# Performance work log

Measured on AMD Instinct MI355X. Metric: run time of the kernel, lower is better.

Reference implementation:

```python
import jax, jax.numpy as jnp
import numpy as np
import math

D_MODEL = 1024
NUM_HEADS = 16
D_K = D_MODEL // NUM_HEADS  # 64
THETA = 10000.0
B, S = 2, 2048


def setup_inputs() -> dict:
    key = jax.random.key(0)
    kx, kq, kk, kv, ko = jax.random.split(key, 5)
    sigma = (2.0 / (D_MODEL + D_MODEL)) ** 0.5
    return {
        "x": jax.random.normal(kx, (B, S, D_MODEL), dtype=jnp.float32),
        "Wq": jax.random.normal(kq, (D_MODEL, D_MODEL), dtype=jnp.float32) * sigma,
        "Wk": jax.random.normal(kk, (D_MODEL, D_MODEL), dtype=jnp.float32) * sigma,
        "Wv": jax.random.normal(kv, (D_MODEL, D_MODEL), dtype=jnp.float32) * sigma,
        "Wo": jax.random.normal(ko, (D_MODEL, D_MODEL), dtype=jnp.float32) * sigma,
        "token_positions": jnp.arange(S, dtype=jnp.int32),
    }


def _rope(x, token_positions):
    # x: [..., seq, d_k]; rotate interleaved even/odd pairs.
    half = x.shape[-1] // 2
    freq = jnp.power(THETA, -jnp.arange(0, x.shape[-1], 2, dtype=jnp.float32) / x.shape[-1])  # [half]
    angles = token_positions[:, None].astype(jnp.float32) * freq[None, :]  # [seq, half]
    cos, sin = jnp.cos(angles), jnp.sin(angles)
    x1 = x[..., 0::2]
    x2 = x[..., 1::2]
    out = jnp.stack([x1 * cos - x2 * sin, x1 * sin + x2 * cos], axis=-1)  # [..., seq, half, 2]
    return out.reshape(x.shape)


def reference(x, Wq, Wk, Wv, Wo, token_positions):
    Bb, Ss, Dm = x.shape
    H, Dk = NUM_HEADS, D_K
    # Linear: y = x @ W.T ; split as (n head) -> heads first
    def heads(y):
        return y.reshape(Bb, Ss, H, Dk).transpose(0, 2, 1, 3)  # [B,H,S,Dk]
    Q = heads(x @ Wq.T)
    K = heads(x @ Wk.T)
    V = heads(x @ Wv.T)
    Q = _rope(Q, token_positions)
    K = _rope(K, token_positions)
    scores = jnp.einsum("bhqd,bhkd->bhqk", Q, K) / math.sqrt(Dk)  # [B,H,S,S]
    causal = jnp.tril(jnp.ones((Ss, Ss), dtype=bool))
    scores = jnp.where(causal, scores, -jnp.inf)
    # original casts to fp64 for softmax; numerically-stable fp32 softmax here
    probs = jax.nn.softmax(scores, axis=-1)
    attn = jnp.einsum("bhqk,bhkd->bhqd", probs, V)  # [B,H,S,Dk]
    attn = attn.transpose(0, 2, 1, 3).reshape(Bb, Ss, Dm)
    return attn @ Wo.T
```

## Files before the change

### kernel.cpp

```cpp
#include <hip/hip_runtime.h>
#include <hip/hip_bf16.h>
#include <math.h>

typedef __bf16 bf16_t;
typedef __attribute__((ext_vector_type(8))) __bf16 bf16x8;
typedef __attribute__((ext_vector_type(4))) __bf16 bf16x4;
typedef __attribute__((ext_vector_type(4))) float f32x4;

#define B_DIM 2
#define S_DIM 2048
#define H_DIM 16
#define DK 64
#define DM 1024
#define KDIM 1024

#define MFMA(a, b, c) __builtin_amdgcn_mfma_f32_16x16x32_bf16((a), (b), (c), 0, 0, 0)

__device__ __forceinline__ void gload_lds16(const bf16_t* g, bf16_t* l) {
    __builtin_amdgcn_global_load_lds(
        (const __attribute__((address_space(1))) void*)g,
        (__attribute__((address_space(3))) void*)l, 16, 0, 0);
}

__global__ void cvt_all(const float* __restrict__ x,
                        const float* __restrict__ wq, const float* __restrict__ wk,
                        const float* __restrict__ wv, const float* __restrict__ wo,
                        bf16_t* __restrict__ xb,
                        bf16_t* __restrict__ wqb, bf16_t* __restrict__ wkb,
                        bf16_t* __restrict__ wvb, bf16_t* __restrict__ wob) {
    const long NX = (long)B_DIM * S_DIM * DM;
    const long i = ((long)blockIdx.x * 256 + threadIdx.x) * 4;
    const float* s; bf16_t* d; long off;
    if (i < NX) { s = x; d = xb; off = i; }
    else {
        const long j = i - NX;
        const int wsel = (int)(j >> 20);
        off = j & ((1L << 20) - 1);
        switch (wsel) {
            case 0: s = wq; d = wqb; break;
            case 1: s = wk; d = wkb; break;
            case 2: s = wv; d = wvb; break;
            default: s = wo; d = wob; break;
        }
    }
    float4 v = *reinterpret_cast<const float4*>(s + off);
    bf16x4 o;
    o[0] = (__bf16)v.x; o[1] = (__bf16)v.y; o[2] = (__bf16)v.z; o[3] = (__bf16)v.w;
    *reinterpret_cast<bf16x4*>(d + off) = o;
}

template <int MODE>
__global__ __launch_bounds__(256)
void gemm_bt(const bf16_t* __restrict__ A,
             const bf16_t* __restrict__ B0,
             const bf16_t* __restrict__ B1,
             const bf16_t* __restrict__ B2,
             bf16_t* __restrict__ outQ,
             bf16_t* __restrict__ outK,
             bf16_t* __restrict__ outVt,
             float* __restrict__ outF,
             const int* __restrict__ pos) {
    constexpr int CP = 136;
    constexpr int SELEMS = (MODE == 0) ? (128 * CP) : 16384;
    __shared__ bf16_t smem[SELEMS];
    bf16_t* As = smem;
    bf16_t* Bs = smem + 8192;
    bf16_t* Cs = smem;

    const int t = threadIdx.x;
    const int z = blockIdx.z;
    const bf16_t* Bm = (MODE == 0) ? (z == 0 ? B0 : (z == 1 ? B1 : B2)) : B0;

    const int m0 = blockIdx.x * 128;
    const int n0 = blockIdx.y * 128;
    const int lane = t & 63;
    const int w = t >> 6;
    const int wr = w >> 1;
    const int wc = w & 1;

    f32x4 acc[4][4] = {};

    const bf16_t* Ag = A + (size_t)m0 * KDIM;
    const bf16_t* Bg = Bm + (size_t)n0 * KDIM;

    const int rr = lane & 15;
    const int ko = (lane >> 4) * 8;

    int rI[4], cI[4];
#pragma unroll
    for (int c = 0; c < 4; ++c) {
        const int i = t + c * 256;
        rI[c] = i >> 3;
        cI[c] = ((i & 7) ^ (rI[c] & 7)) * 8;
    }

    for (int k0 = 0; k0 < KDIM; k0 += 64) {
#pragma unroll
        for (int c = 0; c < 4; ++c) {
            const int i = t + c * 256;
            gload_lds16(Ag + (size_t)rI[c] * KDIM + k0 + cI[c], &As[i * 8]);
        }
#pragma unroll
        for (int c = 0; c < 4; ++c) {
            const int i = t + c * 256;
            gload_lds16(Bg + (size_t)rI[c] * KDIM + k0 + cI[c], &Bs[i * 8]);
        }
        __syncthreads();

        bf16x8 af[2][4], bfr[2][4];
#pragma unroll
        for (int kk = 0; kk < 2; ++kk) {
#pragma unroll
            for (int m = 0; m < 4; ++m) {
                const int r = wr * 64 + m * 16 + rr;
                af[kk][m] = *reinterpret_cast<const bf16x8*>(
                    &As[r * 64 + ((kk * 32 + ko) ^ ((r & 7) * 8))]);
            }
#pragma unroll
            for (int n = 0; n < 4; ++n) {
                const int r = wc * 64 + n * 16 + rr;
                bfr[kk][n] = *reinterpret_cast<const bf16x8*>(
                    &Bs[r * 64 + ((kk * 32 + ko) ^ ((r & 7) * 8))]);
            }
        }
        __builtin_amdgcn_s_setprio(1);
#pragma unroll
        for (int kk = 0; kk < 2; ++kk)
#pragma unroll
            for (int m = 0; m < 4; ++m)
#pragma unroll
                for (int n = 0; n < 4; ++n)
                    acc[m][n] = MFMA(af[kk][m], bfr[kk][n], acc[m][n]);
        __builtin_amdgcn_s_setprio(0);
        __syncthreads();
    }

    const int rlb = wr * 64 + (lane >> 4) * 4;
    const int clb = wc * 64 + (lane & 15);

    if (MODE == 0) {
        if (z < 2) {
#pragma unroll
            for (int m = 0; m < 4; ++m)
#pragma unroll
                for (int n = 0; n < 4; ++n)
#pragma unroll
                    for (int j = 0; j < 4; ++j)
                        Cs[(rlb + m * 16 + j) * CP + clb + n * 16] = (__bf16)acc[m][n][j];
            __syncthreads();

            bf16_t* dst = (z == 0) ? outQ : outK;
            const int dch = t & 7;
            const int srow = t >> 3;
            float fr[4];
#pragma unroll
            for (int i = 0; i < 4; ++i)
                fr[i] = exp2f((float)(dch * 4 + i) * -0.4152410118609203f);
#pragma unroll
            for (int p = 0; p < 4; ++p) {
                const int s_loc = p * 32 + srow;
                const int gm = m0 + s_loc;
                const int bb = gm >> 11, sg = gm & (S_DIM - 1);
                const float pv = (float)pos[sg];
                float csv[4], snv[4];
#pragma unroll
                for (int i = 0; i < 4; ++i) {
                    const float a = pv * fr[i];
                    csv[i] = cosf(a); snv[i] = sinf(a);
                }
#pragma unroll
                for (int hc = 0; hc < 2; ++hc) {
                    const bf16x8 vv = *reinterpret_cast<const bf16x8*>(
                        &Cs[s_loc * CP + hc * 64 + dch * 8]);
                    bf16x8 ov;
#pragma unroll
                    for (int i = 0; i < 4; ++i) {
                        const float v0 = (float)vv[2 * i], v1 = (float)vv[2 * i + 1];
                        ov[2 * i]     = (__bf16)(v0 * csv[i] - v1 * snv[i]);
                        ov[2 * i + 1] = (__bf16)(v0 * snv[i] + v1 * csv[i]);
                    }
                    const int h = (n0 >> 6) + hc;
                    *reinterpret_cast<bf16x8*>(
                        &dst[((size_t)(bb * H_DIM + h) * S_DIM + sg) * 64 + dch * 8]) = ov;
                }
            }
        } else {
#pragma unroll
            for (int m = 0; m < 4; ++m)
#pragma unroll
                for (int n = 0; n < 4; ++n) {
                    const int cl = clb + n * 16;
                    bf16x4 v4;
#pragma unroll
                    for (int j = 0; j < 4; ++j) v4[j] = (__bf16)acc[m][n][j];
                    *reinterpret_cast<bf16x4*>(&Cs[cl * CP + rlb + m * 16]) = v4;
                }
            __syncthreads();

            const int cl = t >> 1, sh = t & 1;
            const int cg = n0 + cl, h = cg >> 6, d = cg & 63;
            const int bb = m0 >> 11, s0g = m0 & (S_DIM - 1);
            bf16_t* vdst = &outVt[((size_t)(bb * H_DIM + h) * DK + d) * S_DIM + s0g + sh * 64];
#pragma unroll
            for (int i = 0; i < 8; ++i)
                *reinterpret_cast<bf16x8*>(&vdst[i * 8]) =
                    *reinterpret_cast<const bf16x8*>(&Cs[cl * CP + sh * 64 + i * 8]);
        }
    } else {
        const int rbase = m0 + rlb;
        const int cbase = n0 + clb;
#pragma unroll
        for (int m = 0; m < 4; ++m)
#pragma unroll
            for (int n = 0; n < 4; ++n)
#pragma unroll
                for (int j = 0; j < 4; ++j)
                    outF[(size_t)(rbase + m * 16 + j) * DM + cbase + n * 16] = acc[m][n][j];
    }
}

__global__ __launch_bounds__(256, 4)
void attn_kernel(const bf16_t* __restrict__ Q, const bf16_t* __restrict__ Kg,
                 const bf16_t* __restrict__ Vt, bf16_t* __restrict__ O) {
    __shared__ bf16_t Ks[2][64 * 64];
    __shared__ bf16_t Vs[2][64 * 64];
    __shared__ bf16_t P_lds[4][16 * 64];

    const int t = threadIdx.x;
    const int lane = t & 63;
    const int w = t >> 6;
    const int qbo = blockIdx.x >> 5;
    const int qb = 31 - qbo;
    const int bh = blockIdx.x & 31;
    const int q0 = qb * 64 + w * 16;
    const int b = bh >> 4, h = bh & 15;
    const int rr = lane & 15;
    const int hi = lane >> 4;
    const int psw = (rr & 7) * 8;

    const bf16_t* Kbh = Kg + (size_t)bh * S_DIM * DK;
    const bf16_t* Vbh = Vt + (size_t)bh * DK * S_DIM;
    bf16_t* Pw = P_lds[w];

    const int i0 = t, i1 = t + 256;
    const int r0 = i0 >> 3, c0 = ((i0 & 7) ^ (r0 & 7)) * 8;
    const int r1 = i1 >> 3, c1 = ((i1 & 7) ^ (r1 & 7)) * 8;

    const float QSCALE = 0.18033688011112042f;
    const bf16_t* Qp = Q + ((size_t)bh * S_DIM + q0) * DK;
    bf16x8 qf[2];
    qf[0] = *reinterpret_cast<const bf16x8*>(&Qp[rr * DK + hi * 8]);
    qf[1] = *reinterpret_cast<const bf16x8*>(&Qp[rr * DK + 32 + hi * 8]);
#pragma unroll
    for (int i = 0; i < 8; ++i) {
        qf[0][i] = (__bf16)((float)qf[0][i] * QSCALE);
        qf[1][i] = (__bf16)((float)qf[1][i] * QSCALE);
    }

    bf16x8 ones;
#pragma unroll
    for (int i = 0; i < 8; ++i) ones[i] = (__bf16)1.0f;

    f32x4 o[4] = {};
    f32x4 la = {};
    float m = -INFINITY;

    const int nt = qb + 1;

    gload_lds16(Kbh + (size_t)r0 * DK + c0, &Ks[0][i0 * 8]);
    gload_lds16(Kbh + (size_t)r1 * DK + c1, &Ks[0][i1 * 8]);
    gload_lds16(Vbh + (size_t)r0 * S_DIM + c0, &Vs[0][i0 * 8]);
    gload_lds16(Vbh + (size_t)r1 * S_DIM + c1, &Vs[0][i1 * 8]);
    __syncthreads();

    for (int tt = 0; tt < nt; ++tt) {
        const int cur = tt & 1;
        const int kv0 = tt * 64;

        if (tt + 1 < nt) {
            const int kv1 = kv0 + 64;
            bf16_t* Kn = Ks[cur ^ 1];
            bf16_t* Vn = Vs[cur ^ 1];
            gload_lds16(Kbh + (size_t)(kv1 + r0) * DK + c0, &Kn[i0 * 8]);
            gload_lds16(Kbh + (size_t)(kv1 + r1) * DK + c1, &Kn[i1 * 8]);
            gload_lds16(Vbh + (size_t)r0 * S_DIM + kv1 + c0, &Vn[i0 * 8]);
            gload_lds16(Vbh + (size_t)r1 * S_DIM + kv1 + c1, &Vn[i1 * 8]);
        }
        const bf16_t* Kc = Ks[cur];
        const bf16_t* Vc = Vs[cur];

        f32x4 s[4] = {};
        __builtin_amdgcn_s_setprio(1);
#pragma unroll
        for (int t16 = 0; t16 < 4; ++t16) {
            const int r = t16 * 16 + rr;
            const int sw = (r & 7) * 8;
            bf16x8 kf0 = *reinterpret_cast<const bf16x8*>(&Kc[r * 64 + ((hi * 8) ^ sw)]);
            bf16x8 kf1 = *reinterpret_cast<const bf16x8*>(&Kc[r * 64 + ((32 + hi * 8) ^ sw)]);
            s[t16] = MFMA(kf0, qf[0], s[t16]);
            s[t16] = MFMA(kf1, qf[1], s[t16]);
        }
        __builtin_amdgcn_s_setprio(0);

        if (tt == qb) {
            const int qg = q0 + rr;
#pragma unroll
            for (int t16 = 0; t16 < 4; ++t16)
#pragma unroll
                for (int j = 0; j < 4; ++j)
                    if (kv0 + t16 * 16 + hi * 4 + j > qg) s[t16][j] = -INFINITY;
        }

        f32x4 mv = s[0];
#pragma unroll
        for (int t16 = 1; t16 < 4; ++t16) {
            mv[0] = fmaxf(mv[0], s[t16][0]); mv[1] = fmaxf(mv[1], s[t16][1]);
            mv[2] = fmaxf(mv[2], s[t16][2]); mv[3] = fmaxf(mv[3], s[t16][3]);
        }
        const float mloc = fmaxf(fmaxf(mv[0], mv[1]), fmaxf(mv[2], mv[3]));
        if (__any(mloc - m > 8.0f)) {
            float mf = fmaxf(mloc, __shfl_xor(mloc, 16));
            mf = fmaxf(mf, __shfl_xor(mf, 32));
            const float mnew = fmaxf(m, mf);
            const float scale = exp2f(m - mnew);
#pragma unroll
            for (int i = 0; i < 4; ++i) la[i] *= scale;
#pragma unroll
            for (int db = 0; db < 4; ++db)
#pragma unroll
                for (int j = 0; j < 4; ++j) o[db][j] *= scale;
            m = mnew;
        }
#pragma unroll
        for (int t16 = 0; t16 < 4; ++t16) {
            bf16x4 pb;
#pragma unroll
            for (int j = 0; j < 4; ++j) pb[j] = (__bf16)exp2f(s[t16][j] - m);
            *reinterpret_cast<bf16x4*>(&Pw[rr * 64 + ((t16 * 16 + hi * 4) ^ psw)]) = pb;
        }

        bf16x8 pf0 = *reinterpret_cast<const bf16x8*>(&Pw[rr * 64 + ((hi * 8) ^ psw)]);
        bf16x8 pf1 = *reinterpret_cast<const bf16x8*>(&Pw[rr * 64 + ((32 + hi * 8) ^ psw)]);
        __builtin_amdgcn_s_setprio(1);
        la = MFMA(ones, pf0, la);
        la = MFMA(ones, pf1, la);
#pragma unroll
        for (int db = 0; db < 4; ++db) {
            const int vr = db * 16 + rr;
            const int sw = (vr & 7) * 8;
            bf16x8 vf0 = *reinterpret_cast<const bf16x8*>(&Vc[vr * 64 + ((hi * 8) ^ sw)]);
            bf16x8 vf1 = *reinterpret_cast<const bf16x8*>(&Vc[vr * 64 + ((32 + hi * 8) ^ sw)]);
            o[db] = MFMA(vf0, pf0, o[db]);
            o[db] = MFMA(vf1, pf1, o[db]);
        }
        __builtin_amdgcn_s_setprio(0);

        __syncthreads();
    }

    const float linv = 1.0f / la[0];
#pragma unroll
    for (int db = 0; db < 4; ++db) {
        bf16x4 ov;
#pragma unroll
        for (int j = 0; j < 4; ++j) ov[j] = (__bf16)(o[db][j] * linv);
        *reinterpret_cast<bf16x4*>(
            &O[((size_t)(b * S_DIM + q0 + rr)) * DM + h * DK + db * 16 + hi * 4]) = ov;
    }
}

extern "C" void kernel_launch(void* const* d_in, const int* in_sizes, int n_in,
                              void* d_out, int out_size, void* d_ws, size_t ws_size,
                              hipStream_t stream) {
    const float* x  = (const float*)d_in[0];
    const float* Wq = (const float*)d_in[1];
    const float* Wk = (const float*)d_in[2];
    const float* Wv = (const float*)d_in[3];
    const float* Wo = (const float*)d_in[4];
    const int* pos  = (const int*)d_in[5];
    float* out = (float*)d_out;

    char* ws = (char*)d_ws;
    bf16_t* xb  = (bf16_t*)(ws);
    bf16_t* Wqb = (bf16_t*)(ws + (8u << 20));
    bf16_t* Wkb = (bf16_t*)(ws + (10u << 20));
    bf16_t* Wvb = (bf16_t*)(ws + (12u << 20));
    bf16_t* Wob = (bf16_t*)(ws + (14u << 20));
    bf16_t* Qb  = (bf16_t*)(ws + (16u << 20));
    bf16_t* Kb  = (bf16_t*)(ws + (24u << 20));
    bf16_t* Vtb = (bf16_t*)(ws + (32u << 20));
    bf16_t* Ab  = (bf16_t*)(ws);

    const int NX = B_DIM * S_DIM * DM;
    const int NW = DM * DM;
    const int NTOT = NX + 4 * NW;

    cvt_all<<<NTOT / 1024, 256, 0, stream>>>(x, Wq, Wk, Wv, Wo,
                                             xb, Wqb, Wkb, Wvb, Wob);

    gemm_bt<0><<<dim3(32, 8, 3), 256, 0, stream>>>(xb, Wqb, Wkb, Wvb,
                                                   Qb, Kb, Vtb, nullptr, pos);

    attn_kernel<<<B_DIM * H_DIM * 32, 256, 0, stream>>>(Qb, Kb, Vtb, Ab);

    gemm_bt<1><<<dim3(32, 8, 1), 256, 0, stream>>>(Ab, Wob, nullptr, nullptr,
                                                   nullptr, nullptr, nullptr, out, pos);
}
```

Before: 110.0 us.

## Split long causal attention query blocks across two workgroups with combine pass

Query blocks 16-31 now have their KV range split at tile 16 across two workgroups, each writing unnormalized fp32 partial outputs plus max and sum to workspace. A new combine kernel merges the partials with log-sum-exp rescaling into the bf16 attention output. Blocks are ordered so the long halves launch first. The goal is to balance causal work across the grid and cut tail latency, at the cost of extra global traffic for partials and an extra kernel launch.

```diff
diff --git a/kernel.cpp b/kernel.cpp
--- a/kernel.cpp
+++ b/kernel.cpp
@@ -221,7 +221,8 @@
 
 __global__ __launch_bounds__(256, 4)
 void attn_kernel(const bf16_t* __restrict__ Q, const bf16_t* __restrict__ Kg,
-                 const bf16_t* __restrict__ Vt, bf16_t* __restrict__ O) {
+                 const bf16_t* __restrict__ Vt, bf16_t* __restrict__ O,
+                 float* __restrict__ Po, float* __restrict__ Pml) {
     __shared__ bf16_t Ks[2][64 * 64];
     __shared__ bf16_t Vs[2][64 * 64];
     __shared__ bf16_t P_lds[4][16 * 64];
@@ -229,9 +230,25 @@
     const int t = threadIdx.x;
     const int lane = t & 63;
     const int w = t >> 6;
-    const int qbo = blockIdx.x >> 5;
-    const int qb = 31 - qbo;
-    const int bh = blockIdx.x & 31;
+    const int bid = blockIdx.x;
+
+    int bh, qb, kvs, kve, slot;
+    bool split;
+    if (bid < 512) {
+        bh = bid & 31; qb = 16 + (bid >> 5);
+        kvs = 0; kve = 16; split = true; slot = (qb - 16) * 32 + bh;
+    } else {
+        const int k = bid - 512;
+        const int g = k >> 5, i = k & 31;
+        if ((g & 1) == 0) {
+            bh = i; qb = 31 - (g >> 1);
+            kvs = 16; kve = qb + 1; split = true; slot = 512 + (qb - 16) * 32 + bh;
+        } else {
+            bh = i; qb = 15 - (g >> 1);
+            kvs = 0; kve = qb + 1; split = false; slot = 0;
+        }
+    }
+
     const int q0 = qb * 64 + w * 16;
     const int b = bh >> 4, h = bh & 15;
     const int rr = lane & 15;
@@ -265,19 +282,17 @@
     f32x4 la = {};
     float m = -INFINITY;
 
-    const int nt = qb + 1;
-
-    gload_lds16(Kbh + (size_t)r0 * DK + c0, &Ks[0][i0 * 8]);
-    gload_lds16(Kbh + (size_t)r1 * DK + c1, &Ks[0][i1 * 8]);
-    gload_lds16(Vbh + (size_t)r0 * S_DIM + c0, &Vs[0][i0 * 8]);
-    gload_lds16(Vbh + (size_t)r1 * S_DIM + c1, &Vs[0][i1 * 8]);
+    gload_lds16(Kbh + (size_t)(kvs * 64 + r0) * DK + c0, &Ks[0][i0 * 8]);
+    gload_lds16(Kbh + (size_t)(kvs * 64 + r1) * DK + c1, &Ks[0][i1 * 8]);
+    gload_lds16(Vbh + (size_t)r0 * S_DIM + kvs * 64 + c0, &Vs[0][i0 * 8]);
+    gload_lds16(Vbh + (size_t)r1 * S_DIM + kvs * 64 + c1, &Vs[0][i1 * 8]);
     __syncthreads();
 
-    for (int tt = 0; tt < nt; ++tt) {
-        const int cur = tt & 1;
+    for (int tt = kvs; tt < kve; ++tt) {
+        const int cur = (tt - kvs) & 1;
         const int kv0 = tt * 64;
 
-        if (tt + 1 < nt) {
+        if (tt + 1 < kve) {
             const int kv1 = kv0 + 64;
             bf16_t* Kn = Ks[cur ^ 1];
             bf16_t* Vn = Vs[cur ^ 1];
@@ -358,15 +373,67 @@
         __syncthreads();
     }
 
-    const float linv = 1.0f / la[0];
-#pragma unroll
-    for (int db = 0; db < 4; ++db) {
-        bf16x4 ov;
-#pragma unroll
-        for (int j = 0; j < 4; ++j) ov[j] = (__bf16)(o[db][j] * linv);
-        *reinterpret_cast<bf16x4*>(
-            &O[((size_t)(b * S_DIM + q0 + rr)) * DM + h * DK + db * 16 + hi * 4]) = ov;
-    }
+    if (!split) {
+        const float linv = 1.0f / la[0];
+#pragma unroll
+        for (int db = 0; db < 4; ++db) {
+            bf16x4 ov;
+#pragma unroll
+            for (int j = 0; j < 4; ++j) ov[j] = (__bf16)(o[db][j] * linv);
+            *reinterpret_cast<bf16x4*>(
+                &O[((size_t)(b * S_DIM + q0 + rr)) * DM + h * DK + db * 16 + hi * 4]) = ov;
+        }
+    } else {
+        const int lrow = w * 16 + rr;
+        float* po = Po + (size_t)slot * 4096 + lrow * 64;
+#pragma unroll
+        for (int db = 0; db < 4; ++db)
+            *reinterpret_cast<f32x4*>(&po[db * 16 + hi * 4]) = o[db];
+        if (hi == 0) {
+            Pml[(size_t)slot * 128 + lrow] = m;
+            Pml[(size_t)slot * 128 + 64 + lrow] = la[0];
+        }
+    }
+}
+
+__global__ __launch_bounds__(256)
+void combine_kernel(const float* __restrict__ Po, const float* __restrict__ Pml,
+                    bf16_t* __restrict__ O) {
+    const int blk = blockIdx.x;
+    const int qb = 16 + (blk >> 5);
+    const int bh = blk & 31;
+    const int b = bh >> 4, h = bh & 15;
+    const int t = threadIdx.x;
+    const int row = t >> 2;
+    const int seg = (t & 3) * 16;
+
+    const int p0 = blk, p1 = 512 + blk;
+    const float m0 = Pml[(size_t)p0 * 128 + row];
+    const float l0 = Pml[(size_t)p0 * 128 + 64 + row];
+    const float m1 = Pml[(size_t)p1 * 128 + row];
+    const float l1 = Pml[(size_t)p1 * 128 + 64 + row];
+    const float M = fmaxf(m0, m1);
+    const float w0 = exp2f(m0 - M), w1 = exp2f(m1 - M);
+    const float inv = 1.0f / (l0 * w0 + l1 * w1);
+
+    const float* o0 = Po + (size_t)p0 * 4096 + row * 64 + seg;
+    const float* o1 = Po + (size_t)p1 * 4096 + row * 64 + seg;
+    bf16_t* dst = &O[((size_t)(b * S_DIM + qb * 64 + row)) * DM + h * DK + seg];
+    bf16x8 ov[2];
+#pragma unroll
+    for (int c = 0; c < 2; ++c) {
+        const f32x4 a0 = *reinterpret_cast<const f32x4*>(o0 + c * 8);
+        const f32x4 b0 = *reinterpret_cast<const f32x4*>(o1 + c * 8);
+        const f32x4 a1 = *reinterpret_cast<const f32x4*>(o0 + c * 8 + 4);
+        const f32x4 b1 = *reinterpret_cast<const f32x4*>(o1 + c * 8 + 4);
+#pragma unroll
+        for (int j = 0; j < 4; ++j) {
+            ov[c][j]     = (__bf16)((a0[j] * w0 + b0[j] * w1) * inv);
+            ov[c][j + 4] = (__bf16)((a1[j] * w0 + b1[j] * w1) * inv);
+        }
+    }
+    *reinterpret_cast<bf16x8*>(dst)     = ov[0];
+    *reinterpret_cast<bf16x8*>(dst + 8) = ov[1];
 }
 
 extern "C" void kernel_launch(void* const* d_in, const int* in_sizes, int n_in,
@@ -390,6 +457,8 @@
     bf16_t* Kb  = (bf16_t*)(ws + (24u << 20));
     bf16_t* Vtb = (bf16_t*)(ws + (32u << 20));
     bf16_t* Ab  = (bf16_t*)(ws);
+    float*  Po  = (float*)(ws + (40u << 20));
+    float*  Pml = (float*)(ws + (56u << 20));
 
     const int NX = B_DIM * S_DIM * DM;
     const int NW = DM * DM;
@@ -401,7 +470,8 @@
     gemm_bt<0><<<dim3(32, 8, 3), 256, 0, stream>>>(xb, Wqb, Wkb, Wvb,
                                                    Qb, Kb, Vtb, nullptr, pos);
 
-    attn_kernel<<<B_DIM * H_DIM * 32, 256, 0, stream>>>(Qb, Kb, Vtb, Ab);
+    attn_kernel<<<1536, 256, 0, stream>>>(Qb, Kb, Vtb, Ab, Po, Pml);
+    combine_kernel<<<512, 256, 0, stream>>>(Po, Pml, Ab);
 
     gemm_bt<1><<<dim3(32, 8, 1), 256, 0, stream>>>(Ab, Wob, nullptr, nullptr,
                                                    nullptr, nullptr, nullptr, out, pos);
```

New measurement: 112.3 us. 1.02x slower.

## Double-buffer GEMM K-tiles with prefetch of next tile during MFMA

Applied to the files above, without the earlier changes.

Restructures the projection GEMM main loop to use a BK=32 double-buffered LDS scheme. The next tile is issued via global_load_lds before computing on the current tile, with a single waitcnt and barrier per iteration. This drops the XOR swizzle, which may introduce LDS bank conflicts on the 64-byte-row layout. It also halves the work per barrier, doubling the iteration count.

```diff
diff --git a/kernel.cpp b/kernel.cpp
--- a/kernel.cpp
+++ b/kernel.cpp
@@ -63,8 +63,6 @@
     constexpr int CP = 136;
     constexpr int SELEMS = (MODE == 0) ? (128 * CP) : 16384;
     __shared__ bf16_t smem[SELEMS];
-    bf16_t* As = smem;
-    bf16_t* Bs = smem + 8192;
     bf16_t* Cs = smem;
 
     const int t = threadIdx.x;
@@ -80,59 +78,55 @@
 
     f32x4 acc[4][4] = {};
 
+    const int ar = t >> 2;
+    const int ac = (t & 3) * 8;
     const bf16_t* Ag = A + (size_t)m0 * KDIM;
     const bf16_t* Bg = Bm + (size_t)n0 * KDIM;
 
     const int rr = lane & 15;
     const int ko = (lane >> 4) * 8;
 
-    int rI[4], cI[4];
-#pragma unroll
-    for (int c = 0; c < 4; ++c) {
-        const int i = t + c * 256;
-        rI[c] = i >> 3;
-        cI[c] = ((i & 7) ^ (rI[c] & 7)) * 8;
-    }
-
-    for (int k0 = 0; k0 < KDIM; k0 += 64) {
-#pragma unroll
-        for (int c = 0; c < 4; ++c) {
-            const int i = t + c * 256;
-            gload_lds16(Ag + (size_t)rI[c] * KDIM + k0 + cI[c], &As[i * 8]);
-        }
-#pragma unroll
-        for (int c = 0; c < 4; ++c) {
-            const int i = t + c * 256;
-            gload_lds16(Bg + (size_t)rI[c] * KDIM + k0 + cI[c], &Bs[i * 8]);
-        }
-        __syncthreads();
-
-        bf16x8 af[2][4], bfr[2][4];
-#pragma unroll
-        for (int kk = 0; kk < 2; ++kk) {
-#pragma unroll
-            for (int m = 0; m < 4; ++m) {
-                const int r = wr * 64 + m * 16 + rr;
-                af[kk][m] = *reinterpret_cast<const bf16x8*>(
-                    &As[r * 64 + ((kk * 32 + ko) ^ ((r & 7) * 8))]);
-            }
-#pragma unroll
-            for (int n = 0; n < 4; ++n) {
-                const int r = wc * 64 + n * 16 + rr;
-                bfr[kk][n] = *reinterpret_cast<const bf16x8*>(
-                    &Bs[r * 64 + ((kk * 32 + ko) ^ ((r & 7) * 8))]);
-            }
-        }
+    constexpr int NT = KDIM / 32;
+
+    gload_lds16(Ag + (size_t)ar * KDIM + ac,        &smem[t * 8]);
+    gload_lds16(Ag + (size_t)(ar + 64) * KDIM + ac, &smem[2048 + t * 8]);
+    gload_lds16(Bg + (size_t)ar * KDIM + ac,        &smem[4096 + t * 8]);
+    gload_lds16(Bg + (size_t)(ar + 64) * KDIM + ac, &smem[6144 + t * 8]);
+    asm volatile("s_waitcnt vmcnt(0)" ::: "memory");
+    __builtin_amdgcn_s_barrier();
+    __builtin_amdgcn_sched_barrier(0);
+
+    for (int it = 0; it < NT; ++it) {
+        const int curo = (it & 1) * 8192;
+        if (it + 1 < NT) {
+            const int nxto = ((it + 1) & 1) * 8192;
+            const int k1 = (it + 1) * 32;
+            gload_lds16(Ag + (size_t)ar * KDIM + k1 + ac,        &smem[nxto + t * 8]);
+            gload_lds16(Ag + (size_t)(ar + 64) * KDIM + k1 + ac, &smem[nxto + 2048 + t * 8]);
+            gload_lds16(Bg + (size_t)ar * KDIM + k1 + ac,        &smem[nxto + 4096 + t * 8]);
+            gload_lds16(Bg + (size_t)(ar + 64) * KDIM + k1 + ac, &smem[nxto + 6144 + t * 8]);
+        }
+
+        const bf16_t* Asc = smem + curo;
+        const bf16_t* Bsc = smem + curo + 4096;
+        bf16x8 af[4], bfr[4];
+#pragma unroll
+        for (int m = 0; m < 4; ++m)
+            af[m] = *reinterpret_cast<const bf16x8*>(&Asc[(wr * 64 + m * 16 + rr) * 32 + ko]);
+#pragma unroll
+        for (int n = 0; n < 4; ++n)
+            bfr[n] = *reinterpret_cast<const bf16x8*>(&Bsc[(wc * 64 + n * 16 + rr) * 32 + ko]);
         __builtin_amdgcn_s_setprio(1);
 #pragma unroll
-        for (int kk = 0; kk < 2; ++kk)
-#pragma unroll
-            for (int m = 0; m < 4; ++m)
-#pragma unroll
-                for (int n = 0; n < 4; ++n)
-                    acc[m][n] = MFMA(af[kk][m], bfr[kk][n], acc[m][n]);
+        for (int m = 0; m < 4; ++m)
+#pragma unroll
+            for (int n = 0; n < 4; ++n)
+                acc[m][n] = MFMA(af[m], bfr[n], acc[m][n]);
         __builtin_amdgcn_s_setprio(0);
-        __syncthreads();
+
+        asm volatile("s_waitcnt vmcnt(0)" ::: "memory");
+        __builtin_amdgcn_s_barrier();
+        __builtin_amdgcn_sched_barrier(0);
     }
 
     const int rlb = wr * 64 + (lane >> 4) * 4;
```

After: 115.5 us. +5.0%, slower.
